# Performance work log

Measured on AMD Instinct MI355X. Metric: run time of the kernel, lower is better.

Reference implementation:

```python
import jax, jax.numpy as jnp
import numpy as np

B, C, H, W = 8, 256, 64, 64
NH = 4
HD = C // NH
EPS_LN = 1e-5
EPS_NORM = 1e-12


def ln2d(x, w, b):
    # LayerNorm over channel dim of NCHW, per spatial location
    m = jnp.mean(x, axis=1, keepdims=True)
    v = jnp.mean((x - m) ** 2, axis=1, keepdims=True)
    return (x - m) / jnp.sqrt(v + EPS_LN) * w[None, :, None, None] + b[None, :, None, None]


def l2norm(x):
    # F.normalize(x, dim=-1)
    n = jnp.sqrt(jnp.sum(x * x, axis=-1, keepdims=True))
    return x / jnp.maximum(n, EPS_NORM)


def setup_inputs() -> dict:
    key = jax.random.key(0)
    ks = jax.random.split(key, 12)
    s = 0.02
    return {
        "img_feat": jax.random.normal(ks[0], (B, C, H, W), jnp.float32),
        "aux0": jax.random.normal(ks[1], (B, C, H, W), jnp.float32),
        "aux1": jax.random.normal(ks[2], (B, C, H, W), jnp.float32),
        "q_ln_w": jnp.ones((C,), jnp.float32),
        "q_ln_b": jnp.zeros((C,), jnp.float32),
        "kv_ln_w": jnp.ones((C,), jnp.float32),
        "kv_ln_b": jnp.zeros((C,), jnp.float32),
        "Wq": jax.random.normal(ks[3], (C, C), jnp.float32) * s,
        "Wkv": jax.random.normal(ks[4], (2 * C, C), jnp.float32) * s,
        "Wo": jax.random.normal(ks[5], (C, C), jnp.float32) * s,
        "bo": jnp.zeros((C,), jnp.float32),
        "attn_scale": jnp.zeros((NH, 1, 1), jnp.float32),
        "mlp_ln_w": jnp.ones((C,), jnp.float32),
        "mlp_ln_b": jnp.zeros((C,), jnp.float32),
        "W1": jax.random.normal(ks[6], (C, C), jnp.float32) * s,
        "b1": jnp.zeros((C,), jnp.float32),
        "W2": jax.random.normal(ks[7], (C, C), jnp.float32) * s,
        "b2": jnp.zeros((C,), jnp.float32),
    }


def reference(img_feat, aux0, aux1, q_ln_w, q_ln_b, kv_ln_w, kv_ln_b,
              Wq, Wkv, Wo, bo, attn_scale, mlp_ln_w, mlp_ln_b, W1, b1, W2, b2):
    HWn = H * W
    # q branch
    q = ln2d(img_feat, q_ln_w, q_ln_b).reshape(B, C, HWn)
    q = jnp.einsum('oc,bcn->bon', Wq, q).reshape(B, NH, HD, HWn)
    # kv branch: cat aux feats along batch (2B)
    kv_in = jnp.concatenate([aux0, aux1], axis=0)
    kv = ln2d(kv_in, kv_ln_w, kv_ln_b).reshape(2 * B, C, HWn)
    kv = jnp.einsum('oc,bcn->bon', Wkv, kv).reshape(2 * B, 2, NH, HD, HWn)
    k, v = kv[:, 0], kv[:, 1]  # each (2B, nh, hd, hw)
    qn = l2norm(q)
    kn = l2norm(k)
    kt, kd = kn[:B], kn[B:]
    vt, vd = v[:B], v[B:]
    # transposed (cross-covariance) cosine attention: hd x hd score matrix
    tex_attn = jax.nn.softmax(jnp.einsum('bnch,bndh->bncd', qn, kt), axis=-1)
    dep_attn = jax.nn.softmax(jnp.einsum('bnch,bndh->bncd', qn, kd), axis=-1)
    tex_qkv = jnp.einsum('bncd,bndh->bnch', tex_attn, vt)
    dep_qkv = jnp.einsum('bncd,bndh->bnch', dep_attn, vd)
    gate = jax.nn.sigmoid(attn_scale)[None]  # (1, nh, 1, 1)
    qkv = gate * tex_qkv + (1.0 - gate) * dep_qkv  # (B, nh, hd, hw)
    qkv = qkv.reshape(B, C, HWn)
    o = jnp.einsum('oc,bcn->bon', Wo, qkv).reshape(B, C, H, W) + bo[None, :, None, None]
    x = img_feat + o
    # ConvMlp (norm_ffn): LayerNorm2d -> 1x1 conv -> GELU -> 1x1 conv
    y = ln2d(x, mlp_ln_w, mlp_ln_b).reshape(B, C, HWn)
    y = jnp.einsum('oc,bcn->bon', W1, y) + b1[None, :, None]
    y = jax.nn.gelu(y)
    y = jnp.einsum('oc,bcn->bon', W2, y) + b2[None, :, None]
    return x + y.reshape(B, C, H, W)
```

## Files before the change

kernel.cpp:

```cpp
#include <hip/hip_runtime.h>
#include <math.h>
#include <stdint.h>

#define B_   8
#define C_   256
#define N_   4096

typedef __bf16 bf16;
typedef __bf16 bf16x8 __attribute__((ext_vector_type(8)));
typedef __bf16 bf16x4 __attribute__((ext_vector_type(4)));
typedef float  f32x4  __attribute__((ext_vector_type(4)));

#define MFMA16(a, b, c) __builtin_amdgcn_mfma_f32_16x16x32_bf16((a), (b), (c), 0, 0, 0)

struct Ptrs { const void* p[18]; };

__device__ __forceinline__ f32x4 ld4(const void* p, long i, bool f32) {
    f32x4 r;
    if (f32) {
        r = *(const f32x4*)((const float*)p + i);
    } else {
        bf16x4 v = *(const bf16x4*)((const bf16*)p + i);
        r[0] = (float)v[0]; r[1] = (float)v[1]; r[2] = (float)v[2]; r[3] = (float)v[3];
    }
    return r;
}

__device__ __forceinline__ float wave_sum(float s) {
    #pragma unroll
    for (int off = 32; off; off >>= 1) s += __shfl_xor(s, off);
    return s;
}

__device__ __forceinline__ void gl_lds16(const bf16* g, bf16* l) {
    __builtin_amdgcn_global_load_lds(
        (const __attribute__((address_space(1))) void*)(uintptr_t)g,
        (__attribute__((address_space(3))) void*)(uintptr_t)l, 16, 0, 0);
}

__global__ __launch_bounds__(256) void prep_kernel(Ptrs a, bf16* __restrict__ wb,
                                                   float* __restrict__ Sbuf,
                                                   bf16* __restrict__ biasb) {
    bool f32 = ((const unsigned*)a.p[3])[0] == 0x3F800000u;
    int row = blockIdx.x * 4 + (threadIdx.x >> 6);
    int lane = threadIdx.x & 63;
    long c4 = lane * 4;
    if (row >= 1536) {
        if (row == 1539) {
            if (lane == 0) {
                f32x4 v = ld4(a.p[11], 0, f32);
                #pragma unroll
                for (int j = 0; j < 4; ++j) biasb[768 + j] = (bf16)v[j];
            }
        } else {
            const void* s = (row == 1536) ? a.p[10] : (row == 1537) ? a.p[15] : a.p[17];
            f32x4 v = ld4(s, c4, f32);
            bf16x4 o;
            #pragma unroll
            for (int j = 0; j < 4; ++j) o[j] = (bf16)v[j];
            *(bf16x4*)(biasb + (row - 1536) * 256 + c4) = o;
        }
        return;
    }
    const void *W, *lw = nullptr, *lb = nullptr;
    long wrow; bf16* dst; float *s1 = nullptr, *s2 = nullptr;
    if (row < 256)       { W = a.p[7];  lw = a.p[3];  lb = a.p[4];  wrow = row;        dst = wb + row * 256;                 s1 = Sbuf + row;          s2 = Sbuf + 256 + row; }
    else if (row < 768)  { W = a.p[8];  lw = a.p[5];  lb = a.p[6];  wrow = row - 256;  dst = wb + 65536 + wrow * 256;        s1 = Sbuf + 512 + wrow;   s2 = Sbuf + 1024 + wrow; }
    else if (row < 1024) { W = a.p[14]; lw = a.p[12]; lb = a.p[13]; wrow = row - 768;  dst = wb + 196608 + wrow * 256;       s1 = Sbuf + 1536 + wrow;  s2 = Sbuf + 1792 + wrow; }
    else if (row < 1280) { W = a.p[9];  wrow = row - 1024; dst = wb + 262144 + wrow * 256; }
    else                 { W = a.p[16]; wrow = row - 1280; dst = wb + 327680 + wrow * 256; }
    f32x4 W4 = ld4(W, wrow * 256 + c4, f32);
    f32x4 w4, b4;
    if (lw) { w4 = ld4(lw, c4, f32); b4 = ld4(lb, c4, f32); }
    else    { w4[0]=w4[1]=w4[2]=w4[3]=1.f; b4[0]=b4[1]=b4[2]=b4[3]=0.f; }
    bf16x4 o;
    float s1v = 0.f, s2v = 0.f;
    #pragma unroll
    for (int j = 0; j < 4; ++j) {
        float wp = W4[j] * w4[j];
        o[j] = (bf16)wp;
        s1v += wp;
        s2v += W4[j] * b4[j];
    }
    *(bf16x4*)(dst + c4) = o;
    if (s1) {
        s1v = wave_sum(s1v); s2v = wave_sum(s2v);
        if (lane == 0) { *s1 = s1v; *s2 = s2v; }
    }
}

__global__ __launch_bounds__(256) void transpose_kernel(Ptrs a, bf16* __restrict__ xT,
                                                        float2* __restrict__ st) {
    bool f32 = ((const unsigned*)a.p[3])[0] == 0x3F800000u;
    int gt = blockIdx.z;
    const void* src; int batch;
    if (gt < 8)       { src = a.p[0]; batch = gt; }
    else if (gt < 16) { src = a.p[1]; batch = gt - 8; }
    else              { src = a.p[2]; batch = gt - 16; }
    int n0 = blockIdx.x * 64;
    int t = threadIdx.x;
    __shared__ bf16 T[64][72];
    int cl = t >> 4, n4 = (t & 15) * 4;
    int c8 = (t & 7) * 8, nl = t >> 3;
    float sa[2] = {0.f, 0.f}, qa[2] = {0.f, 0.f};
    for (int ct = 0; ct < 4; ++ct) {
        int c0 = ct * 64;
        if (ct) __syncthreads();
        #pragma unroll
        for (int i = 0; i < 4; ++i) {
            int c = i * 16 + cl;
            f32x4 v = ld4(src, ((long)batch * 256 + c0 + c) * 4096 + n0 + n4, f32);
            #pragma unroll
            for (int j = 0; j < 4; ++j) T[c][n4 + j] = (bf16)v[j];
        }
        __syncthreads();
        #pragma unroll
        for (int j = 0; j < 2; ++j) {
            int n = j * 32 + nl;
            bf16x8 o;
            #pragma unroll
            for (int jj = 0; jj < 8; ++jj) o[jj] = T[c8 + jj][n];
            *(bf16x8*)(xT + ((size_t)gt * 4096 + n0 + n) * 256 + c0 + c8) = o;
            #pragma unroll
            for (int jj = 0; jj < 8; ++jj) { float f = (float)o[jj]; sa[j] += f; qa[j] += f * f; }
        }
    }
    #pragma unroll
    for (int j = 0; j < 2; ++j) {
        float s = sa[j], q = qa[j];
        #pragma unroll
        for (int off = 1; off < 8; off <<= 1) { s += __shfl_xor(s, off); q += __shfl_xor(q, off); }
        if ((t & 7) == 0) {
            float mean = s * (1.0f / 256.0f);
            float var  = q * (1.0f / 256.0f) - mean * mean;
            float2 o2; o2.x = mean; o2.y = rsqrtf(var + 1e-5f);
            st[(size_t)gt * 4096 + n0 + j * 32 + nl] = o2;
        }
    }
}

__global__ __launch_bounds__(256) void statsT_kernel(const bf16* __restrict__ xT,
                                                     float2* __restrict__ st) {
    int row = blockIdx.x * 4 + (threadIdx.x >> 6);
    int lane = threadIdx.x & 63;
    bf16x4 v = *(const bf16x4*)(xT + (size_t)row * 256 + lane * 4);
    float s = 0.f, q = 0.f;
    #pragma unroll
    for (int j = 0; j < 4; ++j) { float f = (float)v[j]; s += f; q += f * f; }
    s = wave_sum(s); q = wave_sum(q);
    if (lane == 0) {
        float mean = s * (1.0f / 256.0f);
        float var  = q * (1.0f / 256.0f) - mean * mean;
        float2 o; o.x = mean; o.y = rsqrtf(var + 1e-5f);
        st[row] = o;
    }
}

__global__ __launch_bounds__(256, 4) void wgemm_kernel(const bf16* __restrict__ A,
                                                    const bf16* __restrict__ xT,
                                                    const float2* __restrict__ stats,
                                                    const float* __restrict__ S1,
                                                    const float* __restrict__ S2,
                                                    const bf16* __restrict__ bias,
                                                    const bf16* __restrict__ resT,
                                                    void* __restrict__ out,
                                                    bf16* __restrict__ vT,
                                                    const unsigned* __restrict__ probe,
                                                    int emode, int gelu) {
    int n0 = blockIdx.x * 128;
    int ot = blockIdx.y;
    int g  = blockIdx.z;
    int t = threadIdx.x, wv = t >> 6, lane = t & 63;
    int m16 = lane & 15, quad = lane >> 4;
    int wr = wv >> 1, wc = wv & 1;
    int rl = lane >> 3, slot = lane & 7;

    __shared__ bf16 As[128 * 64];
    __shared__ bf16 Bs[128 * 64];

    const bf16* Agbase = A + (size_t)ot * 128 * 256;
    const bf16* Bgbase = xT + ((size_t)g * 4096 + n0) * 256;

    auto stage = [&](int ks) {
        #pragma unroll
        for (int i = 0; i < 4; ++i) {
            int row = wv * 32 + i * 8 + rl;
            int koff = ks * 64 + ((slot ^ (row & 7)) << 3);
            gl_lds16(Agbase + (size_t)row * 256 + koff, &As[(wv * 32 + i * 8) * 64]);
            gl_lds16(Bgbase + (size_t)row * 256 + koff, &Bs[(wv * 32 + i * 8) * 64]);
        }
    };

    f32x4 acc[4][4];
    #pragma unroll
    for (int i = 0; i < 4; ++i)
        #pragma unroll
        for (int j = 0; j < 4; ++j) acc[i][j] = (f32x4){0.f, 0.f, 0.f, 0.f};

    auto compute = [&]() {
        #pragma unroll
        for (int kf = 0; kf < 2; ++kf) {
            bf16x8 af[4], bv[4];
            #pragma unroll
            for (int mt = 0; mt < 4; ++mt) {
                int r = wr * 64 + mt * 16 + m16;
                af[mt] = *(const bf16x8*)&As[r * 64 + (((kf * 4 + quad) ^ (r & 7)) << 3)];
            }
            #pragma unroll
            for (int nt = 0; nt < 4; ++nt) {
                int r = wc * 64 + nt * 16 + m16;
                bv[nt] = *(const bf16x8*)&Bs[r * 64 + (((kf * 4 + quad) ^ (r & 7)) << 3)];
            }
            #pragma unroll
            for (int mt = 0; mt < 4; ++mt)
                #pragma unroll
                for (int nt = 0; nt < 4; ++nt)
                    acc[mt][nt] = MFMA16(af[mt], bv[nt], acc[mt][nt]);
        }
    };

    #pragma unroll
    for (int ks = 0; ks < 4; ++ks) {
        if (ks) __syncthreads();
        stage(ks);
        __syncthreads();
        compute();
    }

    int of32 = (emode == 3) ? (probe[0] == 0x3F800000u) : 0;

    #pragma unroll
    for (int mt = 0; mt < 4; ++mt) {
        int olb  = wr * 64 + mt * 16 + quad * 4;
        int orow = ot * 128 + olb;
        f32x4 s1v, s2v, bz;
        if (stats) { s1v = *(const f32x4*)(S1 + orow); s2v = *(const f32x4*)(S2 + orow); }
        if (bias) {
            bf16x4 bb = *(const bf16x4*)(bias + orow);
            #pragma unroll
            for (int r = 0; r < 4; ++r) bz[r] = (float)bb[r];
        }
        #pragma unroll
        for (int nt = 0; nt < 4; ++nt) {
            int n = n0 + wc * 64 + nt * 16 + m16;
            f32x4 v = acc[mt][nt];
            if (stats) {
                float2 st = stats[(size_t)g * N_ + n];
                float a1 = st.y, a2 = -st.y * st.x;
                #pragma unroll
                for (int r = 0; r < 4; ++r) v[r] = a1 * v[r] + a2 * s1v[r] + s2v[r];
            }
            if (bias) {
                #pragma unroll
                for (int r = 0; r < 4; ++r) v[r] += bz[r];
            }
            if (gelu) {
                #pragma unroll
                for (int r = 0; r < 4; ++r) {
                    float x = v[r];
                    float u = x + 0.044715f * x * x * x;
                    v[r] = 0.5f * x * (1.0f + tanhf(0.7978845608028654f * u));
                }
            }
            if (emode == 0) {
                if (vT == nullptr || orow < 256) {
                    bf16* o = (bf16*)out;
                    #pragma unroll
                    for (int r = 0; r < 4; ++r)
                        o[((size_t)(g * 256 + orow + r)) * N_ + n] = (bf16)v[r];
                } else {
                    int od = orow - 256;
                    int hh = od >> 6, d0 = od & 63;
                    bf16x4 tmp;
                    #pragma unroll
                    for (int r = 0; r < 4; ++r) tmp[r] = (bf16)v[r];
                    *(bf16x4*)(vT + (((size_t)(g * 4 + hh)) * N_ + n) * 64 + d0) = tmp;
                }
            } else if (emode == 2) {
                size_t idx = ((size_t)g * N_ + n) * 256 + orow;
                if (resT) {
                    bf16x4 rr = *(const bf16x4*)(resT + idx);
                    #pragma unroll
                    for (int r = 0; r < 4; ++r) v[r] += (float)rr[r];
                }
                bf16x4 tmp;
                #pragma unroll
                for (int r = 0; r < 4; ++r) tmp[r] = (bf16)v[r];
                *(bf16x4*)((bf16*)out + idx) = tmp;
            } else {
                bf16x4 rr = *(const bf16x4*)(resT + ((size_t)g * N_ + n) * 256 + orow);
                #pragma unroll
                for (int r = 0; r < 4; ++r) {
                    float val = v[r] + (float)rr[r];
                    size_t oi = ((size_t)(g * 256 + orow + r)) * N_ + n;
                    if (of32) ((float*)out)[oi] = val;
                    else      ((bf16*)out)[oi] = (bf16)val;
                }
            }
        }
    }
}

__global__ __launch_bounds__(256) void rownorm_kernel(const bf16* __restrict__ x,
                                                      float* __restrict__ invn) {
    size_t row = blockIdx.x;
    const bf16* p = x + (row << 12);
    int t = threadIdx.x;
    float s = 0.f;
    #pragma unroll
    for (int i = 0; i < 2; ++i) {
        bf16x8 v = *(const bf16x8*)(p + ((size_t)(i * 256 + t) << 3));
        #pragma unroll
        for (int j = 0; j < 8; ++j) { float f = (float)v[j]; s += f * f; }
    }
    #pragma unroll
    for (int off = 32; off > 0; off >>= 1) s += __shfl_down(s, off);
    __shared__ float ps[4];
    if ((t & 63) == 0) ps[t >> 6] = s;
    __syncthreads();
    if (t == 0) {
        float tot = ps[0] + ps[1] + ps[2] + ps[3];
        invn[row] = 1.0f / fmaxf(sqrtf(tot), 1e-12f);
    }
}

__global__ __launch_bounds__(256) void sgemm_kernel(const bf16* __restrict__ q,
                                                    const bf16* __restrict__ k,
                                                    float* __restrict__ Spart) {
    int bh = blockIdx.x, ks = blockIdx.y;
    int b = bh >> 2, h = bh & 3;
    int t = threadIdx.x, wv = t >> 6, lane = t & 63;
    int m16 = lane & 15, quad = lane >> 4;
    const bf16* qrow = q + (size_t)(b * 256 + h * 64 + wv * 16 + m16) * N_;
    const bf16* kt0  = k + (size_t)(b * 256 + h * 64) * N_;
    const bf16* kd0  = k + (size_t)((b + 8) * 256 + h * 64) * N_;

    f32x4 at[4], ad[4];
    #pragma unroll
    for (int i = 0; i < 4; ++i) { at[i] = (f32x4){0.f,0.f,0.f,0.f}; ad[i] = (f32x4){0.f,0.f,0.f,0.f}; }

    int nbeg = ks * 512;
    for (int n = nbeg; n < nbeg + 512; n += 32) {
        int ko = n + quad * 8;
        bf16x8 a = *(const bf16x8*)(qrow + ko);
        #pragma unroll
        for (int dt = 0; dt < 4; ++dt) {
            bf16x8 bt = *(const bf16x8*)(kt0 + (size_t)(dt * 16 + m16) * N_ + ko);
            at[dt] = MFMA16(a, bt, at[dt]);
            bf16x8 bd = *(const bf16x8*)(kd0 + (size_t)(dt * 16 + m16) * N_ + ko);
            ad[dt] = MFMA16(a, bd, ad[dt]);
        }
    }
    float* oT = Spart + (size_t)(ks * 32 + bh) * 4096;
    float* oD = Spart + (size_t)8 * 32 * 4096 + (size_t)(ks * 32 + bh) * 4096;
    #pragma unroll
    for (int dt = 0; dt < 4; ++dt)
        #pragma unroll
        for (int r = 0; r < 4; ++r) {
            int c = wv * 16 + quad * 4 + r, d = dt * 16 + m16;
            oT[c * 64 + d] = at[dt][r];
            oD[c * 64 + d] = ad[dt][r];
        }
}

__global__ __launch_bounds__(256) void softmax_kernel(const float* __restrict__ Spart,
                                                      const float* __restrict__ invnq,
                                                      const float* __restrict__ invnk,
                                                      const bf16* __restrict__ attn_scale,
                                                      bf16* __restrict__ Acat) {
    int bh = blockIdx.x;
    int h = bh & 3;
    int t = threadIdx.x, wv = t >> 6, lane = t & 63;
    float g = 1.0f / (1.0f + expf(-(float)attn_scale[h]));
    #pragma unroll
    for (int i = 0; i < 4; ++i) {
        int idx = blockIdx.y * 16 + wv * 4 + i;
        int stream = idx >> 6, c = idx & 63;
        const float* Sp = Spart + (size_t)stream * 8 * 32 * 4096 + (size_t)bh * 4096 + c * 64 + lane;
        float s = 0.f;
        #pragma unroll
        for (int ks = 0; ks < 8; ++ks) s += Sp[(size_t)ks * 32 * 4096];
        s *= invnq[bh * 64 + c] * invnk[(stream ? bh + 32 : bh) * 64 + lane];
        float mx = s;
        #pragma unroll
        for (int off = 32; off > 0; off >>= 1) mx = fmaxf(mx, __shfl_xor(mx, off));
        float e = expf(s - mx);
        float sum = e;
        #pragma unroll
        for (int off = 32; off > 0; off >>= 1) sum += __shfl_xor(sum, off);
        float a = e / sum * (stream == 0 ? g : 1.0f - g);
        Acat[(size_t)bh * 8192 + c * 128 + stream * 64 + lane] = (bf16)a;
    }
}

__global__ __launch_bounds__(256) void av_kernel(const bf16* __restrict__ Acat,
                                                 const bf16* __restrict__ vT,
                                                 bf16* __restrict__ qkvT) {
    int pt = blockIdx.x, h = blockIdx.y, b = blockIdx.z;
    int bh = b * 4 + h;
    int t = threadIdx.x, wv = t >> 6, lane = t & 63;
    int m16 = lane & 15, quad = lane >> 4;
    int p0 = pt * 64;

    const bf16* Arow = Acat + (size_t)bh * 8192 + (size_t)(wv * 16 + m16) * 128 + quad * 8;
    bf16x8 a[4];
    #pragma unroll
    for (int ds = 0; ds < 4; ++ds) a[ds] = *(const bf16x8*)(Arow + ds * 32);

    f32x4 acc[4];
    #pragma unroll
    for (int i = 0; i < 4; ++i) acc[i] = (f32x4){0.f,0.f,0.f,0.f};

    #pragma unroll
    for (int nt = 0; nt < 4; ++nt) {
        int p = p0 + nt * 16 + m16;
        #pragma unroll
        for (int ds = 0; ds < 4; ++ds) {
            int stream = ds >> 1;
            int dl = (ds & 1) * 32 + quad * 8;
            const bf16* vb = vT + (((size_t)(b + 8 * stream) * 4 + h) * N_ + p) * 64 + dl;
            bf16x8 bv = *(const bf16x8*)vb;
            acc[nt] = MFMA16(a[ds], bv, acc[nt]);
        }
    }
    #pragma unroll
    for (int nt = 0; nt < 4; ++nt) {
        int p = p0 + nt * 16 + m16;
        int cbase = h * 64 + wv * 16 + quad * 4;
        bf16x4 o;
        #pragma unroll
        for (int r = 0; r < 4; ++r) o[r] = (bf16)acc[nt][r];
        *(bf16x4*)(qkvT + ((size_t)b * 4096 + p) * 256 + cbase) = o;
    }
}

extern "C" void kernel_launch(void* const* d_in, const int* in_sizes, int n_in,
                              void* d_out, int out_size, void* d_ws, size_t ws_size,
                              hipStream_t stream) {
    (void)in_sizes; (void)n_in; (void)out_size; (void)ws_size;

    Ptrs args;
    for (int i = 0; i < 18; ++i) args.p[i] = d_in[i];
    const unsigned* probe = (const unsigned*)d_in[3];

    char* ws = (char*)d_ws;
    size_t off = 0;
    auto alloc = [&](size_t bytes) { char* p = ws + off; off += (bytes + 255) & ~(size_t)255; return p; };
    bf16*   xTall = (bf16*)alloc(50331648);
    float2* stAll = (float2*)alloc(786432);
    float2* stX   = (float2*)alloc(262144);
    bf16*   wb    = (bf16*)alloc(786432);
    float*  Sbuf  = (float*)alloc(8192);
    bf16*   biasb = (bf16*)alloc(2048);
    bf16*   q     = (bf16*)alloc(16777216);
    bf16*   k     = (bf16*)alloc(33554432);
    bf16*   vT    = (bf16*)alloc(33554432);
    float*  Spart = (float*)alloc(8388608);
    bf16*   Acat  = (bf16*)alloc(524288);
    float*  invnq = (float*)alloc(8192);
    float*  invnk = (float*)alloc(16384);

    bf16* imgT  = xTall;
    bf16* auxT  = xTall + (size_t)8 * 4096 * 256;
    bf16* qkvT  = q;
    bf16* xbufT = k;
    bf16* h1T   = auxT;

    prep_kernel<<<385, 256, 0, stream>>>(args, wb, Sbuf, biasb);
    transpose_kernel<<<dim3(64, 1, 24), 256, 0, stream>>>(args, xTall, stAll);
    wgemm_kernel<<<dim3(32, 2, 8),  256, 0, stream>>>(wb,         imgT, stAll,            Sbuf,       Sbuf + 256,  nullptr, nullptr, q, nullptr, probe, 0, 0);
    wgemm_kernel<<<dim3(32, 4, 16), 256, 0, stream>>>(wb + 65536, auxT, stAll + 8 * 4096, Sbuf + 512, Sbuf + 1024, nullptr, nullptr, k, vT,      probe, 0, 0);
    rownorm_kernel<<<2048, 256, 0, stream>>>(q, invnq);
    rownorm_kernel<<<4096, 256, 0, stream>>>(k, invnk);
    sgemm_kernel<<<dim3(32, 8), 256, 0, stream>>>(q, k, Spart);
    softmax_kernel<<<dim3(32, 8), 256, 0, stream>>>(Spart, invnq, invnk, biasb + 768, Acat);
    av_kernel<<<dim3(64, 4, 8), 256, 0, stream>>>(Acat, vT, qkvT);
    wgemm_kernel<<<dim3(32, 2, 8), 256, 0, stream>>>(wb + 262144, qkvT, nullptr, nullptr, nullptr, biasb, imgT, xbufT, nullptr, probe, 2, 0);
    statsT_kernel<<<8192, 256, 0, stream>>>(xbufT, stX);
    wgemm_kernel<<<dim3(32, 2, 8), 256, 0, stream>>>(wb + 196608, xbufT, stX, Sbuf + 1536, Sbuf + 1792, biasb + 256, nullptr, h1T, nullptr, probe, 2, 1);
    wgemm_kernel<<<dim3(32, 2, 8), 256, 0, stream>>>(wb + 327680, h1T, nullptr, nullptr, nullptr, biasb + 512, xbufT, d_out, nullptr, probe, 3, 0);
}
```

Measured before the change: 383.7 us.

## Double-buffer GEMM LDS staging and make the transpose LDS tile fp32 with swizzle

The weight GEMM now uses two LDS buffers with async global-to-LDS loads issued two k-steps ahead, waiting on vmcnt counters instead of a full sync before each compute. This is meant to overlap global loads with MFMA work. It doubles LDS per block and lowers the launch-bounds occupancy hint from 4 to 2. The transpose kernel now keeps an fp32 tile stored n-major with an XOR swizzle, so readers fetch contiguous f32x4 vectors rather than eight strided bf16 reads, which should reduce LDS bank conflicts.

```diff
diff --git a/kernel.cpp b/kernel.cpp
--- a/kernel.cpp
+++ b/kernel.cpp
@@ -99,9 +99,9 @@
     else              { src = a.p[2]; batch = gt - 16; }
     int n0 = blockIdx.x * 64;
     int t = threadIdx.x;
-    __shared__ bf16 T[64][72];
+    __shared__ float T[64][68];
     int cl = t >> 4, n4 = (t & 15) * 4;
-    int c8 = (t & 7) * 8, nl = t >> 3;
+    int chunk = t & 7, nr = t >> 3;
     float sa[2] = {0.f, 0.f}, qa[2] = {0.f, 0.f};
     for (int ct = 0; ct < 4; ++ct) {
         int c0 = ct * 64;
@@ -111,16 +111,22 @@
             int c = i * 16 + cl;
             f32x4 v = ld4(src, ((long)batch * 256 + c0 + c) * 4096 + n0 + n4, f32);
             #pragma unroll
-            for (int j = 0; j < 4; ++j) T[c][n4 + j] = (bf16)v[j];
+            for (int j = 0; j < 4; ++j) {
+                int nn = n4 + j;
+                T[nn][c ^ (((nn >> 2) & 3) << 3)] = v[j];
+            }
         }
         __syncthreads();
         #pragma unroll
         for (int j = 0; j < 2; ++j) {
-            int n = j * 32 + nl;
+            int n = j * 32 + nr;
+            int cs = (chunk * 8) ^ (((n >> 2) & 3) << 3);
+            const f32x4* p = (const f32x4*)&T[n][cs];
+            f32x4 lo = p[0], hi = p[1];
             bf16x8 o;
             #pragma unroll
-            for (int jj = 0; jj < 8; ++jj) o[jj] = T[c8 + jj][n];
-            *(bf16x8*)(xT + ((size_t)gt * 4096 + n0 + n) * 256 + c0 + c8) = o;
+            for (int jj = 0; jj < 4; ++jj) { o[jj] = (bf16)lo[jj]; o[4 + jj] = (bf16)hi[jj]; }
+            *(bf16x8*)(xT + ((size_t)gt * 4096 + n0 + n) * 256 + c0 + chunk * 8) = o;
             #pragma unroll
             for (int jj = 0; jj < 8; ++jj) { float f = (float)o[jj]; sa[j] += f; qa[j] += f * f; }
         }
@@ -130,11 +136,11 @@
         float s = sa[j], q = qa[j];
         #pragma unroll
         for (int off = 1; off < 8; off <<= 1) { s += __shfl_xor(s, off); q += __shfl_xor(q, off); }
-        if ((t & 7) == 0) {
+        if (chunk == 0) {
             float mean = s * (1.0f / 256.0f);
             float var  = q * (1.0f / 256.0f) - mean * mean;
             float2 o2; o2.x = mean; o2.y = rsqrtf(var + 1e-5f);
-            st[(size_t)gt * 4096 + n0 + j * 32 + nl] = o2;
+            st[(size_t)gt * 4096 + n0 + j * 32 + nr] = o2;
         }
     }
 }
@@ -156,7 +162,7 @@
     }
 }
 
-__global__ __launch_bounds__(256, 4) void wgemm_kernel(const bf16* __restrict__ A,
+__global__ __launch_bounds__(256, 2) void wgemm_kernel(const bf16* __restrict__ A,
                                                     const bf16* __restrict__ xT,
                                                     const float2* __restrict__ stats,
                                                     const float* __restrict__ S1,
@@ -175,19 +181,19 @@
     int wr = wv >> 1, wc = wv & 1;
     int rl = lane >> 3, slot = lane & 7;
 
-    __shared__ bf16 As[128 * 64];
-    __shared__ bf16 Bs[128 * 64];
+    __shared__ bf16 As[2][128 * 64];
+    __shared__ bf16 Bs[2][128 * 64];
 
     const bf16* Agbase = A + (size_t)ot * 128 * 256;
     const bf16* Bgbase = xT + ((size_t)g * 4096 + n0) * 256;
 
-    auto stage = [&](int ks) {
+    auto stage = [&](int buf, int ks) {
         #pragma unroll
         for (int i = 0; i < 4; ++i) {
             int row = wv * 32 + i * 8 + rl;
             int koff = ks * 64 + ((slot ^ (row & 7)) << 3);
-            gl_lds16(Agbase + (size_t)row * 256 + koff, &As[(wv * 32 + i * 8) * 64]);
-            gl_lds16(Bgbase + (size_t)row * 256 + koff, &Bs[(wv * 32 + i * 8) * 64]);
+            gl_lds16(Agbase + (size_t)row * 256 + koff, &As[buf][(wv * 32 + i * 8) * 64]);
+            gl_lds16(Bgbase + (size_t)row * 256 + koff, &Bs[buf][(wv * 32 + i * 8) * 64]);
         }
     };
 
@@ -197,19 +203,19 @@
         #pragma unroll
         for (int j = 0; j < 4; ++j) acc[i][j] = (f32x4){0.f, 0.f, 0.f, 0.f};
 
-    auto compute = [&]() {
+    auto compute = [&](int buf) {
         #pragma unroll
         for (int kf = 0; kf < 2; ++kf) {
             bf16x8 af[4], bv[4];
             #pragma unroll
             for (int mt = 0; mt < 4; ++mt) {
                 int r = wr * 64 + mt * 16 + m16;
-                af[mt] = *(const bf16x8*)&As[r * 64 + (((kf * 4 + quad) ^ (r & 7)) << 3)];
+                af[mt] = *(const bf16x8*)&As[buf][r * 64 + (((kf * 4 + quad) ^ (r & 7)) << 3)];
             }
             #pragma unroll
             for (int nt = 0; nt < 4; ++nt) {
                 int r = wc * 64 + nt * 16 + m16;
-                bv[nt] = *(const bf16x8*)&Bs[r * 64 + (((kf * 4 + quad) ^ (r & 7)) << 3)];
+                bv[nt] = *(const bf16x8*)&Bs[buf][r * 64 + (((kf * 4 + quad) ^ (r & 7)) << 3)];
             }
             #pragma unroll
             for (int mt = 0; mt < 4; ++mt)
@@ -219,12 +225,17 @@
         }
     };
 
+    stage(0, 0);
+    stage(1, 1);
     #pragma unroll
     for (int ks = 0; ks < 4; ++ks) {
-        if (ks) __syncthreads();
-        stage(ks);
-        __syncthreads();
-        compute();
+        if (ks < 3) asm volatile("s_waitcnt vmcnt(8)" ::: "memory");
+        else        asm volatile("s_waitcnt vmcnt(0)" ::: "memory");
+        __builtin_amdgcn_sched_barrier(0);
+        __builtin_amdgcn_s_barrier();
+        compute(ks & 1);
+        __builtin_amdgcn_s_barrier();
+        if (ks < 2) stage(ks & 1, ks + 2);
     }
 
     int of32 = (emode == 3) ? (probe[0] == 0x3F800000u) : 0;
```

New measurement: 382.1 us. No clear change (-0.4%).
